# Kernel tuning notes

Measured on AMD Instinct MI355X. Metric: run time of the kernel, lower is better.

## Reference

```python
import jax, jax.numpy as jnp
import numpy as np


def setup_inputs() -> dict:
    key = jax.random.key(0)
    k1, k2, k3 = jax.random.split(key, 3)
    B, Lq, Lk, D = 8, 512, 512, 64
    q = jax.random.normal(k1, (B, Lq, D), dtype=jnp.float32)
    k = jax.random.normal(k2, (B, Lk, D), dtype=jnp.float32)
    v = jax.random.normal(k3, (B, Lk, D), dtype=jnp.float32)
    return {"q": q, "k": k, "v": v}


def reference(q, k, v):
    scale = 1.0
    # broadcast add: [B, Lq, 1, D] + [B, 1, Lk, D] -> [B, Lq, Lk, D]
    scores = jnp.sum(scale * jnp.tanh(q[:, :, None, :] + k[:, None, :, :]), axis=-1)  # [B, Lq, Lk]
    attn = jax.nn.softmax(scores, axis=-1)
    out = jnp.einsum('bqk,bkd->bqd', attn, v)
    return out
```

## Files before the change

### kernel.cpp

```cpp
#include <hip/hip_runtime.h>

namespace {
constexpr int Bn = 8, LQ = 512, LK = 512, Dn = 64;
constexpr int QT = 8, KT = 128, NT = LK / KT;
constexpr float C2 = 2.8853900817779268f;

__global__ __launch_bounds__(256, 2)
void addattn(const float* __restrict__ Q, const float* __restrict__ K,
             const float* __restrict__ V, float* __restrict__ O)
{
  __shared__ __align__(16) float ek[KT][Dn + 1];
  __shared__ __align__(16) float eqs[QT][Dn];
  __shared__ __align__(16) float pl[QT][KT + 4];
  __shared__ float lsum[QT];

  const int t  = threadIdx.x;
  const int bb = blockIdx.x >> 6;
  const int q0 = (blockIdx.x & 63) * QT;

  if (t < 128) {
    const int r = t >> 4, d4 = t & 15;
    float4 qv = *(const float4*)(Q + ((bb * LQ + q0 + r) * Dn) + d4 * 4);
    float4 e;
    e.x = __builtin_amdgcn_exp2f(qv.x * C2);
    e.y = __builtin_amdgcn_exp2f(qv.y * C2);
    e.z = __builtin_amdgcn_exp2f(qv.z * C2);
    e.w = __builtin_amdgcn_exp2f(qv.w * C2);
    *(float4*)&eqs[r][d4 * 4] = e;
  }
  if (t < QT) lsum[t] = 0.f;
  __syncthreads();

  float ac0 = 0.f, ac1 = 0.f, ac2 = 0.f, ac3 = 0.f;

  const int kk   = t & 127;
  const int qg   = (t >> 7) * 4;
  const int rr   = (t >> 4) & 7;
  const int dq   = t & 15;
  const int half = t >> 7;

  for (int tile = 0; tile < NT; ++tile) {
    const int k0 = tile * KT;

    #pragma unroll
    for (int pass = 0; pass < 8; ++pass) {
      const int f = t + 256 * pass;
      const int sk = f >> 4, sd = f & 15;
      float4 kv = *(const float4*)(K + ((bb * LK + k0 + sk) * Dn) + sd * 4);
      ek[sk][sd * 4 + 0] = __builtin_amdgcn_exp2f(kv.x * C2);
      ek[sk][sd * 4 + 1] = __builtin_amdgcn_exp2f(kv.y * C2);
      ek[sk][sd * 4 + 2] = __builtin_amdgcn_exp2f(kv.z * C2);
      ek[sk][sd * 4 + 3] = __builtin_amdgcn_exp2f(kv.w * C2);
    }
    __syncthreads();

    {
      float a0 = 0.f, a1 = 0.f, a2 = 0.f, a3 = 0.f;
      #pragma unroll
      for (int d4 = 0; d4 < 16; ++d4) {
        const float4 e0 = *(const float4*)&eqs[qg + 0][d4 * 4];
        const float4 e1 = *(const float4*)&eqs[qg + 1][d4 * 4];
        const float4 e2 = *(const float4*)&eqs[qg + 2][d4 * 4];
        const float4 e3 = *(const float4*)&eqs[qg + 3][d4 * 4];
        const float x0 = ek[kk][d4 * 4 + 0];
        const float x1 = ek[kk][d4 * 4 + 1];
        const float x2 = ek[kk][d4 * 4 + 2];
        const float x3 = ek[kk][d4 * 4 + 3];
        a0 += __builtin_amdgcn_rcpf(fmaf(e0.x, x0, 1.f));
        a1 += __builtin_amdgcn_rcpf(fmaf(e1.x, x0, 1.f));
        a2 += __builtin_amdgcn_rcpf(fmaf(e2.x, x0, 1.f));
        a3 += __builtin_amdgcn_rcpf(fmaf(e3.x, x0, 1.f));
        a0 += __builtin_amdgcn_rcpf(fmaf(e0.y, x1, 1.f));
        a1 += __builtin_amdgcn_rcpf(fmaf(e1.y, x1, 1.f));
        a2 += __builtin_amdgcn_rcpf(fmaf(e2.y, x1, 1.f));
        a3 += __builtin_amdgcn_rcpf(fmaf(e3.y, x1, 1.f));
        a0 += __builtin_amdgcn_rcpf(fmaf(e0.z, x2, 1.f));
        a1 += __builtin_amdgcn_rcpf(fmaf(e1.z, x2, 1.f));
        a2 += __builtin_amdgcn_rcpf(fmaf(e2.z, x2, 1.f));
        a3 += __builtin_amdgcn_rcpf(fmaf(e3.z, x2, 1.f));
        a0 += __builtin_amdgcn_rcpf(fmaf(e0.w, x3, 1.f));
        a1 += __builtin_amdgcn_rcpf(fmaf(e1.w, x3, 1.f));
        a2 += __builtin_amdgcn_rcpf(fmaf(e2.w, x3, 1.f));
        a3 += __builtin_amdgcn_rcpf(fmaf(e3.w, x3, 1.f));
      }
      pl[qg + 0][kk] = __builtin_amdgcn_exp2f(-C2 * a0);
      pl[qg + 1][kk] = __builtin_amdgcn_exp2f(-C2 * a1);
      pl[qg + 2][kk] = __builtin_amdgcn_exp2f(-C2 * a2);
      pl[qg + 3][kk] = __builtin_amdgcn_exp2f(-C2 * a3);
    }
    __syncthreads();

    {
      const int r = t >> 5, c = t & 31;
      float4 p4 = *(const float4*)&pl[r][c * 4];
      float s = (p4.x + p4.y) + (p4.z + p4.w);
      s += __shfl_xor(s, 1);
      s += __shfl_xor(s, 2);
      s += __shfl_xor(s, 4);
      s += __shfl_xor(s, 8);
      s += __shfl_xor(s, 16);
      if (c == 0) lsum[r] += s;
    }

    {
      const float* vb = V + ((bb * LK + k0 + half * 64) * Dn) + dq * 4;
      const float* prow = &pl[rr][half * 64];
      #pragma unroll 8
      for (int j = 0; j < 64; ++j) {
        float4 v4 = *(const float4*)(vb + j * Dn);
        float pw = prow[j];
        ac0 = fmaf(pw, v4.x, ac0);
        ac1 = fmaf(pw, v4.y, ac1);
        ac2 = fmaf(pw, v4.z, ac2);
        ac3 = fmaf(pw, v4.w, ac3);
      }
    }
    __syncthreads();
  }

  if (half == 1) {
    *(float4*)&eqs[rr][dq * 4] = make_float4(ac0, ac1, ac2, ac3);
  }
  __syncthreads();
  if (half == 0) {
    float4 o = *(const float4*)&eqs[rr][dq * 4];
    float inv = 1.0f / lsum[rr];
    float4 r;
    r.x = (ac0 + o.x) * inv;
    r.y = (ac1 + o.y) * inv;
    r.z = (ac2 + o.z) * inv;
    r.w = (ac3 + o.w) * inv;
    *(float4*)(O + ((bb * LQ + q0 + rr) * Dn) + dq * 4) = r;
  }
}
}

extern "C" void kernel_launch(void* const* d_in, const int* in_sizes, int n_in,
                              void* d_out, int out_size, void* d_ws, size_t ws_size,
                              hipStream_t stream) {
  (void)in_sizes; (void)n_in; (void)d_ws; (void)ws_size; (void)out_size;
  const float* Q = (const float*)d_in[0];
  const float* K = (const float*)d_in[1];
  const float* V = (const float*)d_in[2];
  float* O = (float*)d_out;
  addattn<<<dim3(Bn * (LQ / QT)), dim3(256), 0, stream>>>(Q, K, V, O);
}
```

Measured before the change: 90.42 us.

## Double-buffer K tiles through registers with 512 threads and 256-key tiles

Block size goes to 512 threads and the key tile to 256. The next K tile is prefetched into registers while the current tile is scored, and its exp is written to LDS only after the PV step, which removes one barrier per tile. Row sums are now reduced across the wavefront and added with LDS atomics. PV partials are split across 8 key segments with two query rows per thread and reduced through LDS at the end. Costs are higher register pressure from the kv prefetch array, a larger LDS footprint, and a launch bound of 4 that may cause spills.

New measurement: 95.90 us. +6.1%, slower.

```diff
diff --git a/kernel.cpp b/kernel.cpp
--- a/kernel.cpp
+++ b/kernel.cpp
@@ -2,10 +2,10 @@
 
 namespace {
 constexpr int Bn = 8, LQ = 512, LK = 512, Dn = 64;
-constexpr int QT = 8, KT = 128, NT = LK / KT;
+constexpr int T = 512, QT = 8, KT = 256, NT = LK / KT;
 constexpr float C2 = 2.8853900817779268f;
 
-__global__ __launch_bounds__(256, 2)
+__global__ __launch_bounds__(T, 4)
 void addattn(const float* __restrict__ Q, const float* __restrict__ K,
              const float* __restrict__ V, float* __restrict__ O)
 {
@@ -29,39 +29,49 @@
     *(float4*)&eqs[r][d4 * 4] = e;
   }
   if (t < QT) lsum[t] = 0.f;
+
+  const int sk_ = t >> 4, sd_ = t & 15;
+  float4 kv[8];
+  const float* kbase = K + (bb * LK) * Dn + sd_ * 4;
+
+  #pragma unroll
+  for (int p = 0; p < 8; ++p)
+    kv[p] = *(const float4*)(kbase + (p * 32 + sk_) * Dn);
+  #pragma unroll
+  for (int p = 0; p < 8; ++p) {
+    const int row = p * 32 + sk_;
+    ek[row][sd_ * 4 + 0] = __builtin_amdgcn_exp2f(kv[p].x * C2);
+    ek[row][sd_ * 4 + 1] = __builtin_amdgcn_exp2f(kv[p].y * C2);
+    ek[row][sd_ * 4 + 2] = __builtin_amdgcn_exp2f(kv[p].z * C2);
+    ek[row][sd_ * 4 + 3] = __builtin_amdgcn_exp2f(kv[p].w * C2);
+  }
   __syncthreads();
 
-  float ac0 = 0.f, ac1 = 0.f, ac2 = 0.f, ac3 = 0.f;
-
-  const int kk   = t & 127;
-  const int qg   = (t >> 7) * 4;
-  const int rr   = (t >> 4) & 7;
-  const int dq   = t & 15;
-  const int half = t >> 7;
+  const int kk = t & 255;
+  const int qb = (t >> 8) * 4;
+  const int dq  = t & 15;
+  const int rg  = (t >> 4) & 3;
+  const int seg = t >> 6;
+  float ac00 = 0.f, ac01 = 0.f, ac02 = 0.f, ac03 = 0.f;
+  float ac10 = 0.f, ac11 = 0.f, ac12 = 0.f, ac13 = 0.f;
 
   for (int tile = 0; tile < NT; ++tile) {
     const int k0 = tile * KT;
 
-    #pragma unroll
-    for (int pass = 0; pass < 8; ++pass) {
-      const int f = t + 256 * pass;
-      const int sk = f >> 4, sd = f & 15;
-      float4 kv = *(const float4*)(K + ((bb * LK + k0 + sk) * Dn) + sd * 4);
-      ek[sk][sd * 4 + 0] = __builtin_amdgcn_exp2f(kv.x * C2);
-      ek[sk][sd * 4 + 1] = __builtin_amdgcn_exp2f(kv.y * C2);
-      ek[sk][sd * 4 + 2] = __builtin_amdgcn_exp2f(kv.z * C2);
-      ek[sk][sd * 4 + 3] = __builtin_amdgcn_exp2f(kv.w * C2);
+    if (tile + 1 < NT) {
+      #pragma unroll
+      for (int p = 0; p < 8; ++p)
+        kv[p] = *(const float4*)(kbase + (k0 + KT + p * 32 + sk_) * Dn);
     }
-    __syncthreads();
 
     {
       float a0 = 0.f, a1 = 0.f, a2 = 0.f, a3 = 0.f;
       #pragma unroll
       for (int d4 = 0; d4 < 16; ++d4) {
-        const float4 e0 = *(const float4*)&eqs[qg + 0][d4 * 4];
-        const float4 e1 = *(const float4*)&eqs[qg + 1][d4 * 4];
-        const float4 e2 = *(const float4*)&eqs[qg + 2][d4 * 4];
-        const float4 e3 = *(const float4*)&eqs[qg + 3][d4 * 4];
+        const float4 e0 = *(const float4*)&eqs[qb + 0][d4 * 4];
+        const float4 e1 = *(const float4*)&eqs[qb + 1][d4 * 4];
+        const float4 e2 = *(const float4*)&eqs[qb + 2][d4 * 4];
+        const float4 e3 = *(const float4*)&eqs[qb + 3][d4 * 4];
         const float x0 = ek[kk][d4 * 4 + 0];
         const float x1 = ek[kk][d4 * 4 + 1];
         const float x2 = ek[kk][d4 * 4 + 2];
@@ -83,54 +93,81 @@
         a2 += __builtin_amdgcn_rcpf(fmaf(e2.w, x3, 1.f));
         a3 += __builtin_amdgcn_rcpf(fmaf(e3.w, x3, 1.f));
       }
-      pl[qg + 0][kk] = __builtin_amdgcn_exp2f(-C2 * a0);
-      pl[qg + 1][kk] = __builtin_amdgcn_exp2f(-C2 * a1);
-      pl[qg + 2][kk] = __builtin_amdgcn_exp2f(-C2 * a2);
-      pl[qg + 3][kk] = __builtin_amdgcn_exp2f(-C2 * a3);
+      const float p0 = __builtin_amdgcn_exp2f(-C2 * a0);
+      const float p1 = __builtin_amdgcn_exp2f(-C2 * a1);
+      const float p2 = __builtin_amdgcn_exp2f(-C2 * a2);
+      const float p3 = __builtin_amdgcn_exp2f(-C2 * a3);
+      pl[qb + 0][kk] = p0;
+      pl[qb + 1][kk] = p1;
+      pl[qb + 2][kk] = p2;
+      pl[qb + 3][kk] = p3;
+
+      float s0 = p0, s1 = p1, s2 = p2, s3 = p3;
+      #pragma unroll
+      for (int m = 1; m < 64; m <<= 1) {
+        s0 += __shfl_xor(s0, m);
+        s1 += __shfl_xor(s1, m);
+        s2 += __shfl_xor(s2, m);
+        s3 += __shfl_xor(s3, m);
+      }
+      if ((t & 63) == 0) {
+        atomicAdd(&lsum[qb + 0], s0);
+        atomicAdd(&lsum[qb + 1], s1);
+        atomicAdd(&lsum[qb + 2], s2);
+        atomicAdd(&lsum[qb + 3], s3);
+      }
     }
     __syncthreads();
 
     {
-      const int r = t >> 5, c = t & 31;
-      float4 p4 = *(const float4*)&pl[r][c * 4];
-      float s = (p4.x + p4.y) + (p4.z + p4.w);
-      s += __shfl_xor(s, 1);
-      s += __shfl_xor(s, 2);
-      s += __shfl_xor(s, 4);
-      s += __shfl_xor(s, 8);
-      s += __shfl_xor(s, 16);
-      if (c == 0) lsum[r] += s;
+      const float* vb   = V + ((bb * LK + k0 + seg * 32) * Dn) + dq * 4;
+      const float* pr0  = &pl[2 * rg + 0][seg * 32];
+      const float* pr1  = &pl[2 * rg + 1][seg * 32];
+      #pragma unroll 8
+      for (int j = 0; j < 32; ++j) {
+        float4 v4 = *(const float4*)(vb + j * Dn);
+        float pa = pr0[j], pb = pr1[j];
+        ac00 = fmaf(pa, v4.x, ac00);
+        ac01 = fmaf(pa, v4.y, ac01);
+        ac02 = fmaf(pa, v4.z, ac02);
+        ac03 = fmaf(pa, v4.w, ac03);
+        ac10 = fmaf(pb, v4.x, ac10);
+        ac11 = fmaf(pb, v4.y, ac11);
+        ac12 = fmaf(pb, v4.z, ac12);
+        ac13 = fmaf(pb, v4.w, ac13);
+      }
     }
 
-    {
-      const float* vb = V + ((bb * LK + k0 + half * 64) * Dn) + dq * 4;
-      const float* prow = &pl[rr][half * 64];
-      #pragma unroll 8
-      for (int j = 0; j < 64; ++j) {
-        float4 v4 = *(const float4*)(vb + j * Dn);
-        float pw = prow[j];
-        ac0 = fmaf(pw, v4.x, ac0);
-        ac1 = fmaf(pw, v4.y, ac1);
-        ac2 = fmaf(pw, v4.z, ac2);
-        ac3 = fmaf(pw, v4.w, ac3);
+    if (tile + 1 < NT) {
+      #pragma unroll
+      for (int p = 0; p < 8; ++p) {
+        const int row = p * 32 + sk_;
+        ek[row][sd_ * 4 + 0] = __builtin_amdgcn_exp2f(kv[p].x * C2);
+        ek[row][sd_ * 4 + 1] = __builtin_amdgcn_exp2f(kv[p].y * C2);
+        ek[row][sd_ * 4 + 2] = __builtin_amdgcn_exp2f(kv[p].z * C2);
+        ek[row][sd_ * 4 + 3] = __builtin_amdgcn_exp2f(kv[p].w * C2);
       }
     }
     __syncthreads();
   }
 
-  if (half == 1) {
-    *(float4*)&eqs[rr][dq * 4] = make_float4(ac0, ac1, ac2, ac3);
-  }
+  float* scr = &ek[0][0];
+  *(float4*)(scr + ((seg * 8 + 2 * rg + 0) * 64) + dq * 4) =
+      make_float4(ac00, ac01, ac02, ac03);
+  *(float4*)(scr + ((seg * 8 + 2 * rg + 1) * 64) + dq * 4) =
+      make_float4(ac10, ac11, ac12, ac13);
   __syncthreads();
-  if (half == 0) {
-    float4 o = *(const float4*)&eqs[rr][dq * 4];
-    float inv = 1.0f / lsum[rr];
-    float4 r;
-    r.x = (ac0 + o.x) * inv;
-    r.y = (ac1 + o.y) * inv;
-    r.z = (ac2 + o.z) * inv;
-    r.w = (ac3 + o.w) * inv;
-    *(float4*)(O + ((bb * LQ + q0 + rr) * Dn) + dq * 4) = r;
+  if (t < 128) {
+    const int row = t >> 4, d4 = t & 15;
+    float4 o = make_float4(0.f, 0.f, 0.f, 0.f);
+    #pragma unroll
+    for (int s = 0; s < 8; ++s) {
+      float4 c = *(const float4*)(scr + ((s * 8 + row) * 64) + d4 * 4);
+      o.x += c.x; o.y += c.y; o.z += c.z; o.w += c.w;
+    }
+    const float inv = 1.0f / lsum[row];
+    o.x *= inv; o.y *= inv; o.z *= inv; o.w *= inv;
+    *(float4*)(O + ((bb * LQ + q0 + row) * Dn) + d4 * 4) = o;
   }
 }
 }
@@ -143,5 +180,5 @@
   const float* K = (const float*)d_in[1];
   const float* V = (const float*)d_in[2];
   float* O = (float*)d_out;
-  addattn<<<dim3(Bn * (LQ / QT)), dim3(256), 0, stream>>>(Q, K, V, O);
+  addattn<<<dim3(Bn * (LQ / QT)), dim3(T), 0, stream>>>(Q, K, V, O);
 }
```

## Double-buffer K/V tiles with async LDS loads and one wave per query row

Applied to the files above, without the earlier changes.

Grows the block to 512 threads and halves the key tile to 64. Each wave now owns one query row, so its probabilities and row sums are reduced with wave shuffles instead of a block-wide pass. V tiles are copied straight into LDS with global_load_lds, and the next K tile is prefetched into registers and exponentiated into a second buffer while the current tile is computed. This cuts each tile's three barriers to one and overlaps memory traffic with the rcp-heavy score loop. The cost is more LDS, a cross-wave partial-sum reduction at the end, and reliance on the barrier waiting for the async LDS copies to finish.

After: 80.99 us. 10.4% less time.

```diff
diff --git a/kernel.cpp b/kernel.cpp
--- a/kernel.cpp
+++ b/kernel.cpp
@@ -2,25 +2,41 @@
 
 namespace {
 constexpr int Bn = 8, LQ = 512, LK = 512, Dn = 64;
-constexpr int QT = 8, KT = 128, NT = LK / KT;
+constexpr int T = 512, QT = 8, KT = 64, NT = LK / KT;
 constexpr float C2 = 2.8853900817779268f;
 
-__global__ __launch_bounds__(256, 2)
+__device__ __forceinline__ void gload_lds16(const float* g, float* l) {
+  __builtin_amdgcn_global_load_lds(
+      (const __attribute__((address_space(1))) void*)g,
+      (__attribute__((address_space(3))) void*)l, 16, 0, 0);
+}
+
+__global__ __launch_bounds__(T, 4)
 void addattn(const float* __restrict__ Q, const float* __restrict__ K,
              const float* __restrict__ V, float* __restrict__ O)
 {
-  __shared__ __align__(16) float ek[KT][Dn + 1];
+  __shared__ __align__(16) float ekL[2][KT][68];
+  __shared__ __align__(16) float vL [2][KT][Dn];
   __shared__ __align__(16) float eqs[QT][Dn];
-  __shared__ __align__(16) float pl[QT][KT + 4];
+  __shared__ __align__(16) float pL [QT][68];
   __shared__ float lsum[QT];
 
-  const int t  = threadIdx.x;
-  const int bb = blockIdx.x >> 6;
-  const int q0 = (blockIdx.x & 63) * QT;
+  const int t    = threadIdx.x;
+  const int w    = t >> 6;
+  const int lane = t & 63;
+  const int ks   = (t >> 4) & 3;
+  const int dq   = t & 15;
+  const int krow = t >> 3;
+  const int kc8  = (t & 7) * 8;
+  const int bb   = blockIdx.x >> 6;
+  const int q0   = (blockIdx.x & 63) * QT;
+
+  const float* Kt = K + (size_t)bb * LK * Dn;
+  const float* Vt = V + (size_t)bb * LK * Dn;
 
   if (t < 128) {
     const int r = t >> 4, d4 = t & 15;
-    float4 qv = *(const float4*)(Q + ((bb * LQ + q0 + r) * Dn) + d4 * 4);
+    float4 qv = *(const float4*)(Q + (size_t)(bb * LQ + q0 + r) * Dn + d4 * 4);
     float4 e;
     e.x = __builtin_amdgcn_exp2f(qv.x * C2);
     e.y = __builtin_amdgcn_exp2f(qv.y * C2);
@@ -28,109 +44,115 @@
     e.w = __builtin_amdgcn_exp2f(qv.w * C2);
     *(float4*)&eqs[r][d4 * 4] = e;
   }
-  if (t < QT) lsum[t] = 0.f;
+  {
+    const float* g = Vt + (size_t)(w * 8) * Dn + lane * 4;
+    float* l = &vL[0][w * 8][0];
+    gload_lds16(g, l);
+    gload_lds16(g + 256, l + 256);
+  }
+  {
+    float4 k0v = *(const float4*)(Kt + (size_t)krow * Dn + kc8);
+    float4 k1v = *(const float4*)(Kt + (size_t)krow * Dn + kc8 + 4);
+    float4 e0, e1;
+    e0.x = __builtin_amdgcn_exp2f(k0v.x * C2);
+    e0.y = __builtin_amdgcn_exp2f(k0v.y * C2);
+    e0.z = __builtin_amdgcn_exp2f(k0v.z * C2);
+    e0.w = __builtin_amdgcn_exp2f(k0v.w * C2);
+    e1.x = __builtin_amdgcn_exp2f(k1v.x * C2);
+    e1.y = __builtin_amdgcn_exp2f(k1v.y * C2);
+    e1.z = __builtin_amdgcn_exp2f(k1v.z * C2);
+    e1.w = __builtin_amdgcn_exp2f(k1v.w * C2);
+    *(float4*)&ekL[0][krow][kc8]     = e0;
+    *(float4*)&ekL[0][krow][kc8 + 4] = e1;
+  }
   __syncthreads();
 
-  float ac0 = 0.f, ac1 = 0.f, ac2 = 0.f, ac3 = 0.f;
-
-  const int kk   = t & 127;
-  const int qg   = (t >> 7) * 4;
-  const int rr   = (t >> 4) & 7;
-  const int dq   = t & 15;
-  const int half = t >> 7;
+  float  dsum = 0.f;
+  float4 acc  = make_float4(0.f, 0.f, 0.f, 0.f);
+  int buf = 0;
 
   for (int tile = 0; tile < NT; ++tile) {
-    const int k0 = tile * KT;
-
-    #pragma unroll
-    for (int pass = 0; pass < 8; ++pass) {
-      const int f = t + 256 * pass;
-      const int sk = f >> 4, sd = f & 15;
-      float4 kv = *(const float4*)(K + ((bb * LK + k0 + sk) * Dn) + sd * 4);
-      ek[sk][sd * 4 + 0] = __builtin_amdgcn_exp2f(kv.x * C2);
-      ek[sk][sd * 4 + 1] = __builtin_amdgcn_exp2f(kv.y * C2);
-      ek[sk][sd * 4 + 2] = __builtin_amdgcn_exp2f(kv.z * C2);
-      ek[sk][sd * 4 + 3] = __builtin_amdgcn_exp2f(kv.w * C2);
+    float4 kv0, kv1;
+    const bool more = (tile + 1 < NT);
+    if (more) {
+      const int kb = (tile + 1) * KT;
+      const float* g = Vt + (size_t)(kb + w * 8) * Dn + lane * 4;
+      float* l = &vL[buf ^ 1][w * 8][0];
+      gload_lds16(g, l);
+      gload_lds16(g + 256, l + 256);
+      kv0 = *(const float4*)(Kt + (size_t)(kb + krow) * Dn + kc8);
+      kv1 = *(const float4*)(Kt + (size_t)(kb + krow) * Dn + kc8 + 4);
     }
-    __syncthreads();
 
     {
       float a0 = 0.f, a1 = 0.f, a2 = 0.f, a3 = 0.f;
+      const float* ekr = &ekL[buf][lane][0];
+      const float* eqr = &eqs[w][0];
       #pragma unroll
       for (int d4 = 0; d4 < 16; ++d4) {
-        const float4 e0 = *(const float4*)&eqs[qg + 0][d4 * 4];
-        const float4 e1 = *(const float4*)&eqs[qg + 1][d4 * 4];
-        const float4 e2 = *(const float4*)&eqs[qg + 2][d4 * 4];
-        const float4 e3 = *(const float4*)&eqs[qg + 3][d4 * 4];
-        const float x0 = ek[kk][d4 * 4 + 0];
-        const float x1 = ek[kk][d4 * 4 + 1];
-        const float x2 = ek[kk][d4 * 4 + 2];
-        const float x3 = ek[kk][d4 * 4 + 3];
-        a0 += __builtin_amdgcn_rcpf(fmaf(e0.x, x0, 1.f));
-        a1 += __builtin_amdgcn_rcpf(fmaf(e1.x, x0, 1.f));
-        a2 += __builtin_amdgcn_rcpf(fmaf(e2.x, x0, 1.f));
-        a3 += __builtin_amdgcn_rcpf(fmaf(e3.x, x0, 1.f));
-        a0 += __builtin_amdgcn_rcpf(fmaf(e0.y, x1, 1.f));
-        a1 += __builtin_amdgcn_rcpf(fmaf(e1.y, x1, 1.f));
-        a2 += __builtin_amdgcn_rcpf(fmaf(e2.y, x1, 1.f));
-        a3 += __builtin_amdgcn_rcpf(fmaf(e3.y, x1, 1.f));
-        a0 += __builtin_amdgcn_rcpf(fmaf(e0.z, x2, 1.f));
-        a1 += __builtin_amdgcn_rcpf(fmaf(e1.z, x2, 1.f));
-        a2 += __builtin_amdgcn_rcpf(fmaf(e2.z, x2, 1.f));
-        a3 += __builtin_amdgcn_rcpf(fmaf(e3.z, x2, 1.f));
-        a0 += __builtin_amdgcn_rcpf(fmaf(e0.w, x3, 1.f));
-        a1 += __builtin_amdgcn_rcpf(fmaf(e1.w, x3, 1.f));
-        a2 += __builtin_amdgcn_rcpf(fmaf(e2.w, x3, 1.f));
-        a3 += __builtin_amdgcn_rcpf(fmaf(e3.w, x3, 1.f));
+        const float4 e = *(const float4*)(eqr + d4 * 4);
+        const float4 x = *(const float4*)(ekr + d4 * 4);
+        a0 += __builtin_amdgcn_rcpf(fmaf(e.x, x.x, 1.f));
+        a1 += __builtin_amdgcn_rcpf(fmaf(e.y, x.y, 1.f));
+        a2 += __builtin_amdgcn_rcpf(fmaf(e.z, x.z, 1.f));
+        a3 += __builtin_amdgcn_rcpf(fmaf(e.w, x.w, 1.f));
       }
-      pl[qg + 0][kk] = __builtin_amdgcn_exp2f(-C2 * a0);
-      pl[qg + 1][kk] = __builtin_amdgcn_exp2f(-C2 * a1);
-      pl[qg + 2][kk] = __builtin_amdgcn_exp2f(-C2 * a2);
-      pl[qg + 3][kk] = __builtin_amdgcn_exp2f(-C2 * a3);
-    }
-    __syncthreads();
-
-    {
-      const int r = t >> 5, c = t & 31;
-      float4 p4 = *(const float4*)&pl[r][c * 4];
-      float s = (p4.x + p4.y) + (p4.z + p4.w);
-      s += __shfl_xor(s, 1);
-      s += __shfl_xor(s, 2);
-      s += __shfl_xor(s, 4);
-      s += __shfl_xor(s, 8);
-      s += __shfl_xor(s, 16);
-      if (c == 0) lsum[r] += s;
+      const float p = __builtin_amdgcn_exp2f(-C2 * ((a0 + a1) + (a2 + a3)));
+      dsum += p;
+      pL[w][lane] = p;
     }
 
     {
-      const float* vb = V + ((bb * LK + k0 + half * 64) * Dn) + dq * 4;
-      const float* prow = &pl[rr][half * 64];
-      #pragma unroll 8
-      for (int j = 0; j < 64; ++j) {
-        float4 v4 = *(const float4*)(vb + j * Dn);
-        float pw = prow[j];
-        ac0 = fmaf(pw, v4.x, ac0);
-        ac1 = fmaf(pw, v4.y, ac1);
-        ac2 = fmaf(pw, v4.z, ac2);
-        ac3 = fmaf(pw, v4.w, ac3);
+      const float* vrow = &vL[buf][ks * 16][dq * 4];
+      const float* prow = &pL[w][ks * 16];
+      #pragma unroll
+      for (int j = 0; j < 16; ++j) {
+        const float4 v4 = *(const float4*)(vrow + j * Dn);
+        const float  pw = prow[j];
+        acc.x = fmaf(pw, v4.x, acc.x);
+        acc.y = fmaf(pw, v4.y, acc.y);
+        acc.z = fmaf(pw, v4.z, acc.z);
+        acc.w = fmaf(pw, v4.w, acc.w);
       }
     }
+
+    if (more) {
+      float4 e0, e1;
+      e0.x = __builtin_amdgcn_exp2f(kv0.x * C2);
+      e0.y = __builtin_amdgcn_exp2f(kv0.y * C2);
+      e0.z = __builtin_amdgcn_exp2f(kv0.z * C2);
+      e0.w = __builtin_amdgcn_exp2f(kv0.w * C2);
+      e1.x = __builtin_amdgcn_exp2f(kv1.x * C2);
+      e1.y = __builtin_amdgcn_exp2f(kv1.y * C2);
+      e1.z = __builtin_amdgcn_exp2f(kv1.z * C2);
+      e1.w = __builtin_amdgcn_exp2f(kv1.w * C2);
+      *(float4*)&ekL[buf ^ 1][krow][kc8]     = e0;
+      *(float4*)&ekL[buf ^ 1][krow][kc8 + 4] = e1;
+    }
+
     __syncthreads();
+    buf ^= 1;
   }
 
-  if (half == 1) {
-    *(float4*)&eqs[rr][dq * 4] = make_float4(ac0, ac1, ac2, ac3);
-  }
+  #pragma unroll
+  for (int m = 1; m < 64; m <<= 1) dsum += __shfl_xor(dsum, m);
+  if (lane == 0) lsum[w] = dsum;
+
+  float* scr = &ekL[0][0][0];
+  *(float4*)(scr + (size_t)(w * 4 + ks) * 64 + dq * 4) = acc;
   __syncthreads();
-  if (half == 0) {
-    float4 o = *(const float4*)&eqs[rr][dq * 4];
-    float inv = 1.0f / lsum[rr];
-    float4 r;
-    r.x = (ac0 + o.x) * inv;
-    r.y = (ac1 + o.y) * inv;
-    r.z = (ac2 + o.z) * inv;
-    r.w = (ac3 + o.w) * inv;
-    *(float4*)(O + ((bb * LQ + q0 + rr) * Dn) + dq * 4) = r;
+
+  if (t < 128) {
+    const int r = t >> 4, d4 = t & 15;
+    float4 o = make_float4(0.f, 0.f, 0.f, 0.f);
+    #pragma unroll
+    for (int s = 0; s < 4; ++s) {
+      const float4 c = *(const float4*)(scr + (size_t)(r * 4 + s) * 64 + d4 * 4);
+      o.x += c.x; o.y += c.y; o.z += c.z; o.w += c.w;
+    }
+    const float inv = 1.0f / lsum[r];
+    o.x *= inv; o.y *= inv; o.z *= inv; o.w *= inv;
+    *(float4*)(O + (size_t)(bb * LQ + q0 + r) * Dn + d4 * 4) = o;
   }
 }
 }
@@ -143,5 +165,5 @@
   const float* K = (const float*)d_in[1];
   const float* V = (const float*)d_in[2];
   float* O = (float*)d_out;
-  addattn<<<dim3(Bn * (LQ / QT)), dim3(256), 0, stream>>>(Q, K, V, O);
+  addattn<<<dim3(Bn * (LQ / QT)), dim3(T), 0, stream>>>(Q, K, V, O);
 }
```
